# Kernel optimization log

Hardware: AMD Instinct MI355X
Metric: run time of the kernel (lower is better)

The kernel has to match this reference:

```python
import jax, jax.numpy as jnp
import numpy as np

C = 512
NUM_HEADS = 8
RF = 4          # reduction_factor
GROUPS = 8      # min(8, C//8)
EPS = 1e-5


def _pos_enc(h, w, c):
    # matches torch _create_positional_encoding; c must be divisible by 4
    y = jnp.arange(h, dtype=jnp.float32)[:, None] * jnp.ones((1, w), jnp.float32)
    x = jnp.ones((h, 1), jnp.float32) * jnp.arange(w, dtype=jnp.float32)[None, :]
    div = jnp.exp(jnp.arange(0, c // 2, 2, dtype=jnp.float32) * (-np.log(10000.0) / (c // 2)))  # [c//4]
    d = div[:, None, None]
    sy, cy = jnp.sin(y[None] * d), jnp.cos(y[None] * d)   # [c//4,h,w]
    sx, cx = jnp.sin(x[None] * d), jnp.cos(x[None] * d)
    pe = jnp.stack([sy, cy, sx, cx], axis=1).reshape(c, h, w)  # interleaved 0::4..3::4
    return pe[None] * 0.01


def _group_norm(x, w, b):
    B, Cc, H, W = x.shape
    g = x.reshape(B, GROUPS, -1)
    m = g.mean(-1, keepdims=True)
    v = g.var(-1, keepdims=True)
    g = (g - m) / jnp.sqrt(v + EPS)
    return g.reshape(B, Cc, H, W) * w[None, :, None, None] + b[None, :, None, None]


def setup_inputs() -> dict:
    key = jax.random.key(0)
    ks = jax.random.split(key, 4)
    B, H, W = 1, 256, 256
    x = jax.random.normal(ks[0], (B, C, H, W), jnp.float32)
    qkv_w = jax.random.normal(ks[1], (3 * C, C), jnp.float32) * 0.02
    proj_w = jax.random.normal(ks[2], (C, C), jnp.float32) * 0.02
    gamma = jax.random.normal(ks[3], (1,), jnp.float32)
    return {
        "x": x,
        "gn_weight": jnp.ones((C,), jnp.float32),
        "gn_bias": jnp.zeros((C,), jnp.float32),
        "qkv_w": qkv_w,
        "proj_w": proj_w,
        "proj_b": jnp.zeros((C,), jnp.float32),
        "gamma": gamma,
        "temperature": jnp.ones((NUM_HEADS, 1, 1), jnp.float32),
    }


def reference(x, gn_weight, gn_bias, qkv_w, proj_w, proj_b, gamma, temperature):
    B, Cc, H, W = x.shape
    hd = Cc // NUM_HEADS
    identity = x
    xn = _group_norm(x, gn_weight, gn_bias)
    # spatial reduction (AvgPool2d k=4 s=4); H,W > 32 in this config
    Hr, Wr = H // RF, W // RF
    xr = xn.reshape(B, Cc, Hr, RF, Wr, RF).mean(axis=(3, 5))
    xr = xr + _pos_enc(Hr, Wr, Cc)
    qkv = jnp.einsum('oc,bchw->bohw', qkv_w, xr)  # 1x1 conv, no bias
    q, k, v = jnp.split(qkv, 3, axis=1)
    N = Hr * Wr
    q = q.reshape(B, NUM_HEADS, hd, N) * (hd ** -0.5) * temperature[None]
    k = k.reshape(B, NUM_HEADS, hd, N)
    v = v.reshape(B, NUM_HEADS, hd, N)
    # chunked attention in torch == plain softmax attention (chunking over queries)
    attn = jax.nn.softmax(jnp.einsum('bhdn,bhdm->bhnm', q, k), axis=-1)
    out = jnp.einsum('bhnm,bhdm->bhdn', attn, v).reshape(B, Cc, Hr, Wr)
    out = jax.image.resize(out, (B, Cc, H, W), method='bilinear')  # align_corners=False
    out = jnp.einsum('oc,bchw->bohw', proj_w, out) + proj_b[None, :, None, None]
    # dropout in eval mode is identity
    return identity + gamma * out
```

## Files before the change

kernel.cpp:

```cpp
#include <hip/hip_runtime.h>
#include <hip/hip_bf16.h>


typedef __attribute__((ext_vector_type(4))) short short4v;
typedef __attribute__((ext_vector_type(8))) short short8v;
typedef __attribute__((ext_vector_type(4))) float f32x4;
typedef __attribute__((ext_vector_type(4))) unsigned int u32x4;

#define MFMA16(a, b, c) __builtin_amdgcn_mfma_f32_16x16x32_bf16(a, b, c, 0, 0, 0)

__device__ __forceinline__ unsigned short bf16r(float f) {
    unsigned int u = __builtin_bit_cast(unsigned int, f);
    u += 0x7fffu + ((u >> 16) & 1u);
    return (unsigned short)(u >> 16);
}
__device__ __forceinline__ float bff(unsigned short s) {
    unsigned int u = ((unsigned int)s) << 16;
    return __builtin_bit_cast(float, u);
}
__device__ __forceinline__ unsigned int fbits(float f) {
    return __builtin_bit_cast(unsigned int, f);
}

typedef const __attribute__((address_space(1))) unsigned int guint;
typedef __attribute__((address_space(3))) unsigned int luint;
__device__ __forceinline__ void gload16(const void* g, void* l) {
    __builtin_amdgcn_global_load_lds((guint*)g, (luint*)l, 16, 0, 0);
}

__global__ __launch_bounds__(256) void k_pool(const float* __restrict__ x,
                                              float* __restrict__ xp,
                                              float* __restrict__ partials,
                                              const float* __restrict__ qkv_w,
                                              const float* __restrict__ proj_w,
                                              const float* __restrict__ temp,
                                              unsigned short* __restrict__ wq_b,
                                              unsigned short* __restrict__ wp_b) {
    if (blockIdx.x >= 64) {
        int idx = ((blockIdx.x - 64) * 512 + blockIdx.y) * 256 + threadIdx.x;
        const int NQ = 1536 * 512;
        const int NTOT = NQ + 512 * 512;
        if (idx < NQ) {
            int o = idx >> 9;
            float sc = (o < 512) ? temp[o >> 6] * 0.125f * 1.44269504f : 1.0f;
            wq_b[idx] = bf16r(qkv_w[idx] * sc);
        } else if (idx < NTOT) {
            wp_b[idx - NQ] = bf16r(proj_w[idx - NQ]);
        }
        return;
    }
    int hr = blockIdx.x;
    int c  = blockIdx.y;
    int t = threadIdx.x;
    int r = t >> 6, wq = t & 63;
    const float4* src = (const float4*)(x + (size_t)c * 65536 + (size_t)(4 * hr + r) * 256 + 4 * wq);
    float4 v = *src;
    float s4 = v.x + v.y + v.z + v.w;
    float q4 = v.x * v.x + v.y * v.y + v.z * v.z + v.w * v.w;

    __shared__ float sm[256];
    __shared__ float wq4[4];
    sm[t] = s4;
    float qq = q4;
#pragma unroll
    for (int off = 1; off < 64; off <<= 1) qq += __shfl_xor(qq, off, 64);
    if ((t & 63) == 0) wq4[t >> 6] = qq;
    __syncthreads();
    if (t < 64) {
        float cs = sm[t] + sm[64 + t] + sm[128 + t] + sm[192 + t];
        xp[(size_t)c * 4096 + hr * 64 + t] = cs * (1.0f / 16.0f);
        float ts = cs;
#pragma unroll
        for (int off = 1; off < 64; off <<= 1) ts += __shfl_xor(ts, off, 64);
        if (t == 0) {
            int g = c >> 6;
            int slot = (c & 63) * 64 + hr;
            partials[(size_t)(g * 4096 + slot) * 2 + 0] = ts;
            partials[(size_t)(g * 4096 + slot) * 2 + 1] = wq4[0] + wq4[1] + wq4[2] + wq4[3];
        }
    }
}

__global__ __launch_bounds__(256) void k_stats(const float* __restrict__ partials,
                                               float* __restrict__ gstats) {
    int g = blockIdx.x;
    int t = threadIdx.x;
    float s = 0.f, q = 0.f;
    for (int i = t; i < 4096; i += 256) {
        s += partials[(size_t)(g * 4096 + i) * 2 + 0];
        q += partials[(size_t)(g * 4096 + i) * 2 + 1];
    }
#pragma unroll
    for (int off = 1; off < 64; off <<= 1) {
        s += __shfl_xor(s, off, 64);
        q += __shfl_xor(q, off, 64);
    }
    __shared__ float ss[4], qs[4];
    if ((t & 63) == 0) { ss[t >> 6] = s; qs[t >> 6] = q; }
    __syncthreads();
    if (t == 0) {
        float S = ss[0] + ss[1] + ss[2] + ss[3];
        float Q = qs[0] + qs[1] + qs[2] + qs[3];
        const float inv = 1.0f / 4194304.0f;
        float m = S * inv;
        float var = Q * inv - m * m;
        gstats[2 * g] = m;
        gstats[2 * g + 1] = rsqrtf(var + 1e-5f);
    }
}

__global__ __launch_bounds__(256) void k_xr(const float* __restrict__ xp,
                                            const float* __restrict__ gs,
                                            const float* __restrict__ gw,
                                            const float* __restrict__ gb,
                                            unsigned short* __restrict__ xr) {
    int idx = blockIdx.x * 256 + threadIdx.x;
    int c = idx >> 12, n = idx & 4095;
    int hr = n >> 6, wr = n & 63;
    int g = c >> 6;
    float m = gs[2 * g], rs = gs[2 * g + 1];
    float xn = (xp[idx] - m) * rs * gw[c] + gb[c];
    int i = c >> 2, kind = c & 3;
    float di = expf(-(float)i * 0.07195578415606394f);
    float arg = ((kind < 2) ? (float)hr : (float)wr) * di;
    float pe = 0.01f * ((kind & 1) ? cosf(arg) : sinf(arg));
    xr[idx] = bf16r(xn + pe);
}

__global__ __launch_bounds__(256) void k_gemm(const unsigned short* __restrict__ A,
                                              const unsigned short* __restrict__ B,
                                              unsigned short* __restrict__ C) {
    __shared__ unsigned short As[128][36];
    __shared__ unsigned short Bs[128][36];
    int t = threadIdx.x;
    int w = t >> 6, l = t & 63, l15 = l & 15, lg = l >> 4;
    int wrow = w >> 1, wcol = w & 1;
    int m0 = blockIdx.y * 128, n0 = blockIdx.x * 128;
    f32x4 acc[4][4] = {};

    for (int k0 = 0; k0 < 512; k0 += 32) {
#pragma unroll
        for (int i = 0; i < 4; i++) {
            int idx = t + 256 * i;
            int row = idx >> 3, kc = idx & 7;
            short4v av = *(const short4v*)(A + (size_t)(m0 + row) * 512 + k0 + 4 * kc);
            *(short4v*)&As[row][4 * kc] = av;
        }
#pragma unroll
        for (int i = 0; i < 4; i++) {
            int idx = t + 256 * i;
            int kr = idx >> 5, nc = idx & 31;
            short4v bv = *(const short4v*)(B + (size_t)(k0 + kr) * 4096 + n0 + 4 * nc);
#pragma unroll
            for (int j = 0; j < 4; j++) Bs[4 * nc + j][kr] = (unsigned short)bv[j];
        }
        __syncthreads();

        short8v af[4];
#pragma unroll
        for (int mi = 0; mi < 4; mi++) {
            int ar = wrow * 64 + mi * 16 + l15;
            short4v a0 = *(const short4v*)&As[ar][4 * lg];
            short4v a1 = *(const short4v*)&As[ar][16 + 4 * lg];
            af[mi] = __builtin_shufflevector(a0, a1, 0, 1, 2, 3, 4, 5, 6, 7);
        }
#pragma unroll
        for (int ni = 0; ni < 4; ni++) {
            int bc = wcol * 64 + ni * 16 + l15;
            short4v b0 = *(const short4v*)&Bs[bc][4 * lg];
            short4v b1 = *(const short4v*)&Bs[bc][16 + 4 * lg];
            short8v bf = __builtin_shufflevector(b0, b1, 0, 1, 2, 3, 4, 5, 6, 7);
#pragma unroll
            for (int mi = 0; mi < 4; mi++) acc[mi][ni] = MFMA16(af[mi], bf, acc[mi][ni]);
        }
        __syncthreads();
    }
#pragma unroll
    for (int mi = 0; mi < 4; mi++)
#pragma unroll
        for (int ni = 0; ni < 4; ni++) {
            int row = m0 + wrow * 64 + mi * 16 + 4 * lg;
            int col = n0 + wcol * 64 + ni * 16 + l15;
#pragma unroll
            for (int r = 0; r < 4; r++)
                C[(size_t)(row + r) * 4096 + col] = bf16r(acc[mi][ni][r]);
        }
}

__global__ __launch_bounds__(256) void k_gemmT(const unsigned short* __restrict__ A,
                                               const unsigned short* __restrict__ BT,
                                               unsigned short* __restrict__ C) {
    __shared__ unsigned short As[128][36];
    __shared__ unsigned short Bs[128][36];
    int t = threadIdx.x;
    int w = t >> 6, l = t & 63, l15 = l & 15, lg = l >> 4;
    int wrow = w >> 1, wcol = w & 1;
    int m0 = blockIdx.y * 128, n0 = blockIdx.x * 128;
    f32x4 acc[4][4] = {};

    for (int k0 = 0; k0 < 512; k0 += 32) {
#pragma unroll
        for (int i = 0; i < 4; i++) {
            int idx = t + 256 * i;
            int row = idx >> 3, kc = idx & 7;
            short4v av = *(const short4v*)(A + (size_t)(m0 + row) * 512 + k0 + 4 * kc);
            *(short4v*)&As[row][4 * kc] = av;
            short4v bv = *(const short4v*)(BT + (size_t)(n0 + row) * 512 + k0 + 4 * kc);
            *(short4v*)&Bs[row][4 * kc] = bv;
        }
        __syncthreads();

        short8v af[4];
#pragma unroll
        for (int mi = 0; mi < 4; mi++) {
            int ar = wrow * 64 + mi * 16 + l15;
            short4v a0 = *(const short4v*)&As[ar][4 * lg];
            short4v a1 = *(const short4v*)&As[ar][16 + 4 * lg];
            af[mi] = __builtin_shufflevector(a0, a1, 0, 1, 2, 3, 4, 5, 6, 7);
        }
#pragma unroll
        for (int ni = 0; ni < 4; ni++) {
            int bc = wcol * 64 + ni * 16 + l15;
            short4v b0 = *(const short4v*)&Bs[bc][4 * lg];
            short4v b1 = *(const short4v*)&Bs[bc][16 + 4 * lg];
            short8v bf = __builtin_shufflevector(b0, b1, 0, 1, 2, 3, 4, 5, 6, 7);
#pragma unroll
            for (int mi = 0; mi < 4; mi++) acc[mi][ni] = MFMA16(af[mi], bf, acc[mi][ni]);
        }
        __syncthreads();
    }
#pragma unroll
    for (int mi = 0; mi < 4; mi++)
#pragma unroll
        for (int ni = 0; ni < 4; ni++) {
            int row = m0 + wrow * 64 + mi * 16 + 4 * lg;
            int col = n0 + wcol * 64 + ni * 16 + l15;
#pragma unroll
            for (int r = 0; r < 4; r++)
                C[(size_t)(row + r) * 4096 + col] = bf16r(acc[mi][ni][r]);
        }
}

__global__ __launch_bounds__(256) void k_perm(const unsigned short* __restrict__ qkv,
                                              unsigned short* __restrict__ qtg,
                                              unsigned short* __restrict__ ktg,
                                              unsigned short* __restrict__ vtg) {
    __shared__ unsigned short lt[64][72];
    int t = threadIdx.x;
    int tile = blockIdx.x, h = blockIdx.y, z = blockIdx.z;
    int base = (z == 0 ? 0 : (z == 1 ? 512 : 1024)) + h * 64;
#pragma unroll
    for (int i = 0; i < 2; i++) {
        int idx = t + 256 * i;
        int row = idx >> 3, sg = idx & 7;
        *(short8v*)&lt[row][sg * 8] =
            *(const short8v*)(qkv + (size_t)(base + row) * 4096 + tile * 64 + sg * 8);
    }
    __syncthreads();
#pragma unroll
    for (int i = 0; i < 2; i++) {
        int c = t + 256 * i;
        unsigned short o[8];
        unsigned short* dst;
        if (z == 0) {
            int nh = c >> 8, cl = c & 255;
            int s = cl >> 7, lgc = (cl >> 5) & 3, col = cl & 31;
#pragma unroll
            for (int j = 0; j < 4; j++) {
                o[j] = lt[s * 32 + 4 * lgc + j][nh * 32 + col];
                o[4 + j] = lt[s * 32 + 16 + 4 * lgc + j][nh * 32 + col];
            }
            dst = qtg + ((size_t)(h * 128 + tile * 2 + nh)) * 2048 + cl * 8;
        } else if (z == 1) {
            int s = c >> 8, lgc = (c >> 6) & 3, m = c & 63;
#pragma unroll
            for (int j = 0; j < 4; j++) {
                o[j] = lt[s * 32 + 4 * lgc + j][m];
                o[4 + j] = lt[s * 32 + 16 + 4 * lgc + j][m];
            }
            dst = ktg + ((size_t)(h * 64 + tile)) * 4096 + c * 8;
        } else {
            int mh = c >> 8, lgc = (c >> 6) & 3, d = c & 63;
#pragma unroll
            for (int j = 0; j < 4; j++) {
                o[j] = lt[d][mh * 32 + 4 * lgc + j];
                o[4 + j] = lt[d][mh * 32 + 16 + 4 * lgc + j];
            }
            dst = vtg + ((size_t)(h * 64 + tile)) * 4096 + c * 8;
        }
        *(short8v*)dst = *(const short8v*)o;
    }
}

__global__ __launch_bounds__(256, 5) void k_attn(const unsigned short* __restrict__ qtg,
                                                 const unsigned short* __restrict__ ktg,
                                                 const unsigned short* __restrict__ vtg,
                                                 unsigned short* __restrict__ opart,
                                                 float* __restrict__ lgl) {
    __shared__ __align__(16) unsigned short kbuf[2][4096];
    __shared__ __align__(16) unsigned short vbuf[2][4096];
    int t = threadIdx.x;
    int l = t & 63, l15 = l & 15, lg = l >> 4, w = t >> 6;
    int qt = blockIdx.x, h = blockIdx.y, seg = blockIdx.z;
    int nu = qt * 4 + w;

    const unsigned short* qb = qtg + ((size_t)(h * 128 + nu)) * 2048;
    const unsigned short* kb = ktg + ((size_t)(h * 64 + seg * 8)) * 4096;
    const unsigned short* vb = vtg + ((size_t)(h * 64 + seg * 8)) * 4096;

    short8v qf[2][2];
#pragma unroll
    for (int ng = 0; ng < 2; ng++)
#pragma unroll
        for (int s = 0; s < 2; s++)
            qf[ng][s] = *(const short8v*)(qb + ((s * 4 + lg) * 32 + ng * 16 + l15) * 8);

    f32x4 od[2][4] = {};
    float lsum[2] = {0.f, 0.f};

#define STAGE(kt, b)                                                            \
    {                                                                           \
        gload16(kb + (size_t)(kt) * 4096 + t * 8, &kbuf[b][t * 8]);             \
        gload16(kb + (size_t)(kt) * 4096 + (t + 256) * 8, &kbuf[b][(t + 256) * 8]); \
        gload16(vb + (size_t)(kt) * 4096 + t * 8, &vbuf[b][t * 8]);             \
        gload16(vb + (size_t)(kt) * 4096 + (t + 256) * 8, &vbuf[b][(t + 256) * 8]); \
    }

    STAGE(0, 0);

    int u = 0;
#pragma unroll 1
    for (int j = 0; j < 8; j++) {
        if (j < 7) {
            STAGE(j + 1, u ^ 1);
            asm volatile("s_waitcnt vmcnt(4)" ::: "memory");
        } else {
            asm volatile("s_waitcnt vmcnt(0)" ::: "memory");
        }
        __builtin_amdgcn_s_barrier();
        __builtin_amdgcn_sched_barrier(0);

        const unsigned short* kl = &kbuf[u][0];
        const unsigned short* vl = &vbuf[u][0];

        u32x4 pwA, pwB;
        short8v pb[2][2];
#pragma unroll
        for (int mf = 0; mf < 4; mf++) {
            short8v k0 = *(const short8v*)(kl + ((0 + lg) * 64 + mf * 16 + l15) * 8);
            short8v k1 = *(const short8v*)(kl + ((4 + lg) * 64 + mf * 16 + l15) * 8);
            f32x4 s0 = {}, s1 = {};
            __builtin_amdgcn_s_setprio(1);
            s0 = MFMA16(k0, qf[0][0], s0);
            s0 = MFMA16(k1, qf[0][1], s0);
            s1 = MFMA16(k0, qf[1][0], s1);
            s1 = MFMA16(k1, qf[1][1], s1);
            __builtin_amdgcn_s_setprio(0);
            float p0[4], p1[4];
#pragma unroll
            for (int r = 0; r < 4; r++) {
                p0[r] = __builtin_amdgcn_exp2f(s0[r]);
                p1[r] = __builtin_amdgcn_exp2f(s1[r]);
            }
            lsum[0] += (p0[0] + p0[1]) + (p0[2] + p0[3]);
            lsum[1] += (p1[0] + p1[1]) + (p1[2] + p1[3]);
            if (!(mf & 1)) {
                pwA[0] = __builtin_amdgcn_perm(fbits(p0[1]), fbits(p0[0]), 0x07060302u);
                pwA[1] = __builtin_amdgcn_perm(fbits(p0[3]), fbits(p0[2]), 0x07060302u);
                pwB[0] = __builtin_amdgcn_perm(fbits(p1[1]), fbits(p1[0]), 0x07060302u);
                pwB[1] = __builtin_amdgcn_perm(fbits(p1[3]), fbits(p1[2]), 0x07060302u);
            } else {
                pwA[2] = __builtin_amdgcn_perm(fbits(p0[1]), fbits(p0[0]), 0x07060302u);
                pwA[3] = __builtin_amdgcn_perm(fbits(p0[3]), fbits(p0[2]), 0x07060302u);
                pwB[2] = __builtin_amdgcn_perm(fbits(p1[1]), fbits(p1[0]), 0x07060302u);
                pwB[3] = __builtin_amdgcn_perm(fbits(p1[3]), fbits(p1[2]), 0x07060302u);
                pb[0][mf >> 1] = __builtin_bit_cast(short8v, pwA);
                pb[1][mf >> 1] = __builtin_bit_cast(short8v, pwB);
            }
        }

        __builtin_amdgcn_s_setprio(1);
#pragma unroll
        for (int mh = 0; mh < 2; mh++)
#pragma unroll
            for (int dg = 0; dg < 4; dg++) {
                short8v vf = *(const short8v*)(vl + ((mh * 4 + lg) * 64 + dg * 16 + l15) * 8);
                od[0][dg] = MFMA16(vf, pb[0][mh], od[0][dg]);
                od[1][dg] = MFMA16(vf, pb[1][mh], od[1][dg]);
            }
        __builtin_amdgcn_s_setprio(0);

        __builtin_amdgcn_s_barrier();
        u ^= 1;
    }
#undef STAGE

#pragma unroll
    for (int ng = 0; ng < 2; ng++) {
        lsum[ng] += __shfl_xor(lsum[ng], 16, 64);
        lsum[ng] += __shfl_xor(lsum[ng], 32, 64);
    }

    unsigned short* op = opart + (((size_t)(seg * 8 + h)) * 4096 + nu * 32) * 64;
#pragma unroll
    for (int ng = 0; ng < 2; ng++)
#pragma unroll
        for (int dg = 0; dg < 4; dg++) {
            unsigned short v4[4];
#pragma unroll
            for (int r = 0; r < 4; r++) v4[r] = bf16r(od[ng][dg][r]);
            *(short4v*)(op + (ng * 16 + l15) * 64 + dg * 16 + 4 * lg) = *(const short4v*)v4;
        }
    if (lg == 0) {
#pragma unroll
        for (int ng = 0; ng < 2; ng++)
            lgl[(size_t)(seg * 8 + h) * 4096 + nu * 32 + ng * 16 + l15] = lsum[ng];
    }
}

__global__ __launch_bounds__(256) void k_merge(const unsigned short* __restrict__ opart,
                                               const float* __restrict__ lgl,
                                               unsigned short* __restrict__ attn_bT) {
    int t = threadIdx.x;
    int n = blockIdx.x * 8 + (t >> 5);
    int cid = t & 31;
    int h = cid >> 2, d0 = (cid & 3) * 16;

    float den = 0.f;
    float num[16] = {};
#pragma unroll
    for (int s = 0; s < 8; s++) {
        den += lgl[(size_t)(s * 8 + h) * 4096 + n];
        const unsigned short* row = opart + (((size_t)(s * 8 + h)) * 4096 + n) * 64 + d0;
        short8v a = *(const short8v*)row;
        short8v b = *(const short8v*)(row + 8);
#pragma unroll
        for (int j = 0; j < 8; j++) {
            num[j] += bff((unsigned short)a[j]);
            num[8 + j] += bff((unsigned short)b[j]);
        }
    }
    float inv = 1.0f / den;
    unsigned short res[16];
#pragma unroll
    for (int j = 0; j < 16; j++) res[j] = bf16r(num[j] * inv);
    unsigned short* dst = attn_bT + (size_t)n * 512 + h * 64 + d0;
    *(short8v*)dst = *(const short8v*)&res[0];
    *(short8v*)(dst + 8) = *(const short8v*)&res[8];
}

__global__ __launch_bounds__(256) void k_up(const float* __restrict__ x,
                                            const unsigned short* __restrict__ low,
                                            const float* __restrict__ proj_b,
                                            const float* __restrict__ gamma,
                                            float* __restrict__ out) {
    int t = threadIdx.x;
    int hs = t >> 6;
    int hh = blockIdx.x * 4 + hs;
    int c = blockIdx.y;
    int a = t & 63;

    int ph = hh & 3, Ah = hh >> 2;
    int y0 = Ah + ((ph < 2) ? -1 : 0);
    float fy = (ph < 2) ? (0.625f + 0.25f * ph) : (0.125f + 0.25f * (ph - 2));
    int y1 = min(y0 + 1, 63); y0 = max(y0, 0);

    const unsigned short* L0 = low + (size_t)c * 4096 + y0 * 64;
    const unsigned short* L1 = low + (size_t)c * 4096 + y1 * 64;
    int am = max(a - 1, 0), ap = min(a + 1, 63);
    float gy = 1.f - fy;
    float vm = gy * bff(L0[am]) + fy * bff(L1[am]);
    float v0 = gy * bff(L0[a])  + fy * bff(L1[a]);
    float vp = gy * bff(L0[ap]) + fy * bff(L1[ap]);

    float pb = proj_b[c], g = gamma[0];
    size_t idx = (size_t)c * 65536 + (size_t)hh * 256 + a * 4;
    float4 xi = *(const float4*)(x + idx);
    float4 o;
    o.x = xi.x + g * (0.375f * vm + 0.625f * v0 + pb);
    o.y = xi.y + g * (0.125f * vm + 0.875f * v0 + pb);
    o.z = xi.z + g * (0.875f * v0 + 0.125f * vp + pb);
    o.w = xi.w + g * (0.625f * v0 + 0.375f * vp + pb);
    *(float4*)(out + idx) = o;
}

extern "C" void kernel_launch(void* const* d_in, const int* in_sizes, int n_in,
                              void* d_out, int out_size, void* d_ws, size_t ws_size,
                              hipStream_t stream) {
    const float* x     = (const float*)d_in[0];
    const float* gnw   = (const float*)d_in[1];
    const float* gnb   = (const float*)d_in[2];
    const float* qkvw  = (const float*)d_in[3];
    const float* projw = (const float*)d_in[4];
    const float* projb = (const float*)d_in[5];
    const float* gamma = (const float*)d_in[6];
    const float* temp  = (const float*)d_in[7];

    char* ws = (char*)d_ws;
    const size_t MB = 1u << 20;
    float* gstats          = (float*)(ws + 0);
    float* partials        = (float*)(ws + 1024);
    float* xp              = (float*)(ws + 1 * MB);
    unsigned short* qtg    = (unsigned short*)(ws + 1 * MB);
    unsigned short* ktg    = (unsigned short*)(ws + 5 * MB);
    unsigned short* xr_b   = (unsigned short*)(ws + 9 * MB);
    unsigned short* vtg    = (unsigned short*)(ws + 9 * MB);
    unsigned short* wq_b   = (unsigned short*)(ws + 13 * MB);
    unsigned short* wp_b   = (unsigned short*)(ws + 15 * MB);
    unsigned short* qkv_b  = (unsigned short*)(ws + 16 * MB);
    unsigned short* attn_bT= (unsigned short*)(ws + 28 * MB);
    unsigned short* low_b  = (unsigned short*)(ws + 32 * MB);
    float* out = (float*)d_out;
    unsigned short* opart = (unsigned short*)d_out;
    float* lgl = (float*)((char*)d_out + 40 * MB);

    k_pool<<<dim3(72, 512), 256, 0, stream>>>(x, xp, partials, qkvw, projw, temp, wq_b, wp_b);
    k_stats<<<8, 256, 0, stream>>>(partials, gstats);
    k_xr<<<8192, 256, 0, stream>>>(xp, gstats, gnw, gnb, xr_b);
    k_gemm<<<dim3(32, 12), 256, 0, stream>>>(wq_b, xr_b, qkv_b);
    k_perm<<<dim3(64, 8, 3), 256, 0, stream>>>(qkv_b, qtg, ktg, vtg);
    k_attn<<<dim3(32, 8, 8), 256, 0, stream>>>(qtg, ktg, vtg, opart, lgl);
    k_merge<<<512, 256, 0, stream>>>(opart, lgl, attn_bT);
    k_gemmT<<<dim3(32, 4), 256, 0, stream>>>(wp_b, attn_bT, low_b);
    k_up<<<dim3(64, 512), 256, 0, stream>>>(x, low_b, projb, gamma, out);
}
```

Before: 185.6 us.

## Fuse QKV permute into GEMM epilogue, halve attention splits, retile proj GEMM

The QKV GEMM now stages its output tile in shared memory and writes Q/K/V straight into the head-permuted layouts, which removes the separate permute kernel and the intermediate qkv buffer round trip. Attention key splits drop from 8 to 4, so each block processes 16 key tiles, and the merge reads fewer partials. The projection GEMM uses 64-row tiles to double its grid. The upsample kernel switches to nontemporal stores. Fewer splits lower attention parallelism in exchange for less merge traffic.

```diff
diff --git a/kernel.cpp b/kernel.cpp
--- a/kernel.cpp
+++ b/kernel.cpp
@@ -127,11 +127,16 @@
     xr[idx] = bf16r(xn + pe);
 }
 
-__global__ __launch_bounds__(256) void k_gemm(const unsigned short* __restrict__ A,
-                                              const unsigned short* __restrict__ B,
-                                              unsigned short* __restrict__ C) {
-    __shared__ unsigned short As[128][36];
-    __shared__ unsigned short Bs[128][36];
+__global__ __launch_bounds__(256) void k_gemmP(const unsigned short* __restrict__ A,
+                                               const unsigned short* __restrict__ B,
+                                               unsigned short* __restrict__ qtg,
+                                               unsigned short* __restrict__ ktg,
+                                               unsigned short* __restrict__ vtg) {
+    __shared__ __align__(16) char smem[33792];
+    unsigned short (*As)[36] = (unsigned short(*)[36])smem;
+    unsigned short (*Bs)[36] = (unsigned short(*)[36])(smem + 9216);
+    unsigned short (*ct)[132] = (unsigned short(*)[132])smem;
+
     int t = threadIdx.x;
     int w = t >> 6, l = t & 63, l15 = l & 15, lg = l >> 4;
     int wrow = w >> 1, wcol = w & 1;
@@ -175,118 +180,55 @@
         }
         __syncthreads();
     }
+
 #pragma unroll
     for (int mi = 0; mi < 4; mi++)
 #pragma unroll
         for (int ni = 0; ni < 4; ni++) {
-            int row = m0 + wrow * 64 + mi * 16 + 4 * lg;
-            int col = n0 + wcol * 64 + ni * 16 + l15;
-#pragma unroll
-            for (int r = 0; r < 4; r++)
-                C[(size_t)(row + r) * 4096 + col] = bf16r(acc[mi][ni][r]);
-        }
-}
-
-__global__ __launch_bounds__(256) void k_gemmT(const unsigned short* __restrict__ A,
-                                               const unsigned short* __restrict__ BT,
-                                               unsigned short* __restrict__ C) {
-    __shared__ unsigned short As[128][36];
-    __shared__ unsigned short Bs[128][36];
-    int t = threadIdx.x;
-    int w = t >> 6, l = t & 63, l15 = l & 15, lg = l >> 4;
-    int wrow = w >> 1, wcol = w & 1;
-    int m0 = blockIdx.y * 128, n0 = blockIdx.x * 128;
-    f32x4 acc[4][4] = {};
-
-    for (int k0 = 0; k0 < 512; k0 += 32) {
-#pragma unroll
-        for (int i = 0; i < 4; i++) {
-            int idx = t + 256 * i;
-            int row = idx >> 3, kc = idx & 7;
-            short4v av = *(const short4v*)(A + (size_t)(m0 + row) * 512 + k0 + 4 * kc);
-            *(short4v*)&As[row][4 * kc] = av;
-            short4v bv = *(const short4v*)(BT + (size_t)(n0 + row) * 512 + k0 + 4 * kc);
-            *(short4v*)&Bs[row][4 * kc] = bv;
-        }
-        __syncthreads();
-
-        short8v af[4];
-#pragma unroll
-        for (int mi = 0; mi < 4; mi++) {
-            int ar = wrow * 64 + mi * 16 + l15;
-            short4v a0 = *(const short4v*)&As[ar][4 * lg];
-            short4v a1 = *(const short4v*)&As[ar][16 + 4 * lg];
-            af[mi] = __builtin_shufflevector(a0, a1, 0, 1, 2, 3, 4, 5, 6, 7);
-        }
-#pragma unroll
-        for (int ni = 0; ni < 4; ni++) {
-            int bc = wcol * 64 + ni * 16 + l15;
-            short4v b0 = *(const short4v*)&Bs[bc][4 * lg];
-            short4v b1 = *(const short4v*)&Bs[bc][16 + 4 * lg];
-            short8v bf = __builtin_shufflevector(b0, b1, 0, 1, 2, 3, 4, 5, 6, 7);
-#pragma unroll
-            for (int mi = 0; mi < 4; mi++) acc[mi][ni] = MFMA16(af[mi], bf, acc[mi][ni]);
-        }
-        __syncthreads();
-    }
-#pragma unroll
-    for (int mi = 0; mi < 4; mi++)
-#pragma unroll
-        for (int ni = 0; ni < 4; ni++) {
-            int row = m0 + wrow * 64 + mi * 16 + 4 * lg;
-            int col = n0 + wcol * 64 + ni * 16 + l15;
-#pragma unroll
-            for (int r = 0; r < 4; r++)
-                C[(size_t)(row + r) * 4096 + col] = bf16r(acc[mi][ni][r]);
-        }
-}
-
-__global__ __launch_bounds__(256) void k_perm(const unsigned short* __restrict__ qkv,
-                                              unsigned short* __restrict__ qtg,
-                                              unsigned short* __restrict__ ktg,
-                                              unsigned short* __restrict__ vtg) {
-    __shared__ unsigned short lt[64][72];
-    int t = threadIdx.x;
-    int tile = blockIdx.x, h = blockIdx.y, z = blockIdx.z;
-    int base = (z == 0 ? 0 : (z == 1 ? 512 : 1024)) + h * 64;
-#pragma unroll
-    for (int i = 0; i < 2; i++) {
-        int idx = t + 256 * i;
-        int row = idx >> 3, sg = idx & 7;
-        *(short8v*)&lt[row][sg * 8] =
-            *(const short8v*)(qkv + (size_t)(base + row) * 4096 + tile * 64 + sg * 8);
-    }
+            int ml = wrow * 64 + mi * 16 + 4 * lg;
+            int nl = wcol * 64 + ni * 16 + l15;
+#pragma unroll
+            for (int r = 0; r < 4; r++) ct[ml + r][nl] = bf16r(acc[mi][ni][r]);
+        }
     __syncthreads();
-#pragma unroll
-    for (int i = 0; i < 2; i++) {
-        int c = t + 256 * i;
+
+    int y = blockIdx.y;
+#pragma unroll
+    for (int i = 0; i < 8; i++) {
+        int gc = t + 256 * i;
+        int hg = gc >> 10, rem = gc & 1023;
         unsigned short o[8];
         unsigned short* dst;
-        if (z == 0) {
-            int nh = c >> 8, cl = c & 255;
-            int s = cl >> 7, lgc = (cl >> 5) & 3, col = cl & 31;
+        if (y < 4) {
+            int nu_loc = rem >> 8, cidx = rem & 255;
+            int s = cidx >> 7, lgc = (cidx >> 5) & 3, col = cidx & 31;
 #pragma unroll
             for (int j = 0; j < 4; j++) {
-                o[j] = lt[s * 32 + 4 * lgc + j][nh * 32 + col];
-                o[4 + j] = lt[s * 32 + 16 + 4 * lgc + j][nh * 32 + col];
+                o[j] = ct[hg * 64 + s * 32 + 4 * lgc + j][nu_loc * 32 + col];
+                o[4 + j] = ct[hg * 64 + s * 32 + 16 + 4 * lgc + j][nu_loc * 32 + col];
             }
-            dst = qtg + ((size_t)(h * 128 + tile * 2 + nh)) * 2048 + cl * 8;
-        } else if (z == 1) {
-            int s = c >> 8, lgc = (c >> 6) & 3, m = c & 63;
+            int h = y * 2 + hg;
+            dst = qtg + ((size_t)(h * 128 + (n0 >> 5) + nu_loc)) * 2048 + cidx * 8;
+        } else if (y < 8) {
+            int Tloc = rem >> 9, cidx = rem & 511;
+            int s = cidx >> 8, lgc = (cidx >> 6) & 3, m64 = cidx & 63;
 #pragma unroll
             for (int j = 0; j < 4; j++) {
-                o[j] = lt[s * 32 + 4 * lgc + j][m];
-                o[4 + j] = lt[s * 32 + 16 + 4 * lgc + j][m];
+                o[j] = ct[hg * 64 + s * 32 + 4 * lgc + j][Tloc * 64 + m64];
+                o[4 + j] = ct[hg * 64 + s * 32 + 16 + 4 * lgc + j][Tloc * 64 + m64];
             }
-            dst = ktg + ((size_t)(h * 64 + tile)) * 4096 + c * 8;
+            int h = (y - 4) * 2 + hg;
+            dst = ktg + ((size_t)(h * 64 + (n0 >> 6) + Tloc)) * 4096 + cidx * 8;
         } else {
-            int mh = c >> 8, lgc = (c >> 6) & 3, d = c & 63;
+            int Tloc = rem >> 9, cidx = rem & 511;
+            int mh = cidx >> 8, lgc = (cidx >> 6) & 3, d = cidx & 63;
 #pragma unroll
             for (int j = 0; j < 4; j++) {
-                o[j] = lt[d][mh * 32 + 4 * lgc + j];
-                o[4 + j] = lt[d][mh * 32 + 16 + 4 * lgc + j];
+                o[j] = ct[hg * 64 + d][Tloc * 64 + mh * 32 + 4 * lgc + j];
+                o[4 + j] = ct[hg * 64 + d][Tloc * 64 + mh * 32 + 16 + 4 * lgc + j];
             }
-            dst = vtg + ((size_t)(h * 64 + tile)) * 4096 + c * 8;
+            int h = (y - 8) * 2 + hg;
+            dst = vtg + ((size_t)(h * 64 + (n0 >> 6) + Tloc)) * 4096 + cidx * 8;
         }
         *(short8v*)dst = *(const short8v*)o;
     }
@@ -305,8 +247,8 @@
     int nu = qt * 4 + w;
 
     const unsigned short* qb = qtg + ((size_t)(h * 128 + nu)) * 2048;
-    const unsigned short* kb = ktg + ((size_t)(h * 64 + seg * 8)) * 4096;
-    const unsigned short* vb = vtg + ((size_t)(h * 64 + seg * 8)) * 4096;
+    const unsigned short* kb = ktg + ((size_t)(h * 64 + seg * 16)) * 4096;
+    const unsigned short* vb = vtg + ((size_t)(h * 64 + seg * 16)) * 4096;
 
     short8v qf[2][2];
 #pragma unroll
@@ -330,8 +272,8 @@
 
     int u = 0;
 #pragma unroll 1
-    for (int j = 0; j < 8; j++) {
-        if (j < 7) {
+    for (int j = 0; j < 16; j++) {
+        if (j < 15) {
             STAGE(j + 1, u ^ 1);
             asm volatile("s_waitcnt vmcnt(4)" ::: "memory");
         } else {
@@ -429,7 +371,7 @@
     float den = 0.f;
     float num[16] = {};
 #pragma unroll
-    for (int s = 0; s < 8; s++) {
+    for (int s = 0; s < 4; s++) {
         den += lgl[(size_t)(s * 8 + h) * 4096 + n];
         const unsigned short* row = opart + (((size_t)(s * 8 + h)) * 4096 + n) * 64 + d0;
         short8v a = *(const short8v*)row;
@@ -447,6 +389,65 @@
     unsigned short* dst = attn_bT + (size_t)n * 512 + h * 64 + d0;
     *(short8v*)dst = *(const short8v*)&res[0];
     *(short8v*)(dst + 8) = *(const short8v*)&res[8];
+}
+
+__global__ __launch_bounds__(256) void k_gemmT(const unsigned short* __restrict__ A,
+                                               const unsigned short* __restrict__ BT,
+                                               unsigned short* __restrict__ C) {
+    __shared__ unsigned short As[64][36];
+    __shared__ unsigned short Bs[128][36];
+    int t = threadIdx.x;
+    int w = t >> 6, l = t & 63, l15 = l & 15, lg = l >> 4;
+    int wrow = w >> 1, wcol = w & 1;
+    int m0 = blockIdx.y * 64, n0 = blockIdx.x * 128;
+    f32x4 acc[2][4] = {};
+
+    for (int k0 = 0; k0 < 512; k0 += 32) {
+#pragma unroll
+        for (int i = 0; i < 2; i++) {
+            int idx = t + 256 * i;
+            int row = idx >> 3, kc = idx & 7;
+            short4v av = *(const short4v*)(A + (size_t)(m0 + row) * 512 + k0 + 4 * kc);
+            *(short4v*)&As[row][4 * kc] = av;
+        }
+#pragma unroll
+        for (int i = 0; i < 4; i++) {
+            int idx = t + 256 * i;
+            int row = idx >> 3, kc = idx & 7;
+            short4v bv = *(const short4v*)(BT + (size_t)(n0 + row) * 512 + k0 + 4 * kc);
+            *(short4v*)&Bs[row][4 * kc] = bv;
+        }
+        __syncthreads();
+
+        short8v af[2];
+#pragma unroll
+        for (int mi = 0; mi < 2; mi++) {
+            int ar = wrow * 32 + mi * 16 + l15;
+            short4v a0 = *(const short4v*)&As[ar][4 * lg];
+            short4v a1 = *(const short4v*)&As[ar][16 + 4 * lg];
+            af[mi] = __builtin_shufflevector(a0, a1, 0, 1, 2, 3, 4, 5, 6, 7);
+        }
+#pragma unroll
+        for (int ni = 0; ni < 4; ni++) {
+            int bc = wcol * 64 + ni * 16 + l15;
+            short4v b0 = *(const short4v*)&Bs[bc][4 * lg];
+            short4v b1 = *(const short4v*)&Bs[bc][16 + 4 * lg];
+            short8v bf = __builtin_shufflevector(b0, b1, 0, 1, 2, 3, 4, 5, 6, 7);
+#pragma unroll
+            for (int mi = 0; mi < 2; mi++) acc[mi][ni] = MFMA16(af[mi], bf, acc[mi][ni]);
+        }
+        __syncthreads();
+    }
+#pragma unroll
+    for (int mi = 0; mi < 2; mi++)
+#pragma unroll
+        for (int ni = 0; ni < 4; ni++) {
+            int row = m0 + wrow * 32 + mi * 16 + 4 * lg;
+            int col = n0 + wcol * 64 + ni * 16 + l15;
+#pragma unroll
+            for (int r = 0; r < 4; r++)
+                C[(size_t)(row + r) * 4096 + col] = bf16r(acc[mi][ni][r]);
+        }
 }
 
 __global__ __launch_bounds__(256) void k_up(const float* __restrict__ x,
@@ -476,12 +477,12 @@
     float pb = proj_b[c], g = gamma[0];
     size_t idx = (size_t)c * 65536 + (size_t)hh * 256 + a * 4;
     float4 xi = *(const float4*)(x + idx);
-    float4 o;
-    o.x = xi.x + g * (0.375f * vm + 0.625f * v0 + pb);
-    o.y = xi.y + g * (0.125f * vm + 0.875f * v0 + pb);
-    o.z = xi.z + g * (0.875f * v0 + 0.125f * vp + pb);
-    o.w = xi.w + g * (0.625f * v0 + 0.375f * vp + pb);
-    *(float4*)(out + idx) = o;
+    f32x4 o;
+    o[0] = xi.x + g * (0.375f * vm + 0.625f * v0 + pb);
+    o[1] = xi.y + g * (0.125f * vm + 0.875f * v0 + pb);
+    o[2] = xi.z + g * (0.875f * v0 + 0.125f * vp + pb);
+    o[3] = xi.w + g * (0.625f * v0 + 0.375f * vp + pb);
+    __builtin_nontemporal_store(o, (f32x4*)(out + idx));
 }
 
 extern "C" void kernel_launch(void* const* d_in, const int* in_sizes, int n_in,
@@ -504,23 +505,21 @@
     unsigned short* qtg    = (unsigned short*)(ws + 1 * MB);
     unsigned short* ktg    = (unsigned short*)(ws + 5 * MB);
     unsigned short* xr_b   = (unsigned short*)(ws + 9 * MB);
-    unsigned short* vtg    = (unsigned short*)(ws + 9 * MB);
-    unsigned short* wq_b   = (unsigned short*)(ws + 13 * MB);
-    unsigned short* wp_b   = (unsigned short*)(ws + 15 * MB);
-    unsigned short* qkv_b  = (unsigned short*)(ws + 16 * MB);
-    unsigned short* attn_bT= (unsigned short*)(ws + 28 * MB);
-    unsigned short* low_b  = (unsigned short*)(ws + 32 * MB);
+    unsigned short* vtg    = (unsigned short*)(ws + 13 * MB);
+    unsigned short* wq_b   = (unsigned short*)(ws + 17 * MB);
+    unsigned short* wp_b   = (unsigned short*)(ws + 19 * MB);
+    unsigned short* attn_bT= (unsigned short*)(ws + 21 * MB);
+    unsigned short* low_b  = (unsigned short*)(ws + 25 * MB);
     float* out = (float*)d_out;
     unsigned short* opart = (unsigned short*)d_out;
-    float* lgl = (float*)((char*)d_out + 40 * MB);
+    float* lgl = (float*)((char*)d_out + 16 * MB);
 
     k_pool<<<dim3(72, 512), 256, 0, stream>>>(x, xp, partials, qkvw, projw, temp, wq_b, wp_b);
     k_stats<<<8, 256, 0, stream>>>(partials, gstats);
     k_xr<<<8192, 256, 0, stream>>>(xp, gstats, gnw, gnb, xr_b);
-    k_gemm<<<dim3(32, 12), 256, 0, stream>>>(wq_b, xr_b, qkv_b);
-    k_perm<<<dim3(64, 8, 3), 256, 0, stream>>>(qkv_b, qtg, ktg, vtg);
-    k_attn<<<dim3(32, 8, 8), 256, 0, stream>>>(qtg, ktg, vtg, opart, lgl);
+    k_gemmP<<<dim3(32, 12), 256, 0, stream>>>(wq_b, xr_b, qtg, ktg, vtg);
+    k_attn<<<dim3(32, 8, 4), 256, 0, stream>>>(qtg, ktg, vtg, opart, lgl);
     k_merge<<<512, 256, 0, stream>>>(opart, lgl, attn_bT);
-    k_gemmT<<<dim3(32, 4), 256, 0, stream>>>(wp_b, attn_bT, low_b);
+    k_gemmT<<<dim3(32, 8), 256, 0, stream>>>(wp_b, attn_bT, low_b);
     k_up<<<dim3(64, 512), 256, 0, stream>>>(x, low_b, projb, gamma, out);
 }
```

New measurement: 179.7 us. 3.2% less time.
